# Performance work log

Hardware: AMD Instinct MI355X
Metric: run time of the kernel (lower is better)

Reference implementation:

```python
import jax, jax.numpy as jnp
import numpy as np

MAX_PER_CLASS = 100   # max_num_boxes_per_class
MAX_TOTAL = 300       # max_num_boxes (pad_per_class=False -> output size is MAX_TOTAL)
IOU_THR = 0.5
SCORE_THR = 0.001
NEG = jnp.float32(-1e30)
EPS = 1e-12


def _canon(b):
    # boxes given as any diagonal pair (y1,x1,y2,x2); canonicalize like TF NMS
    ymin = jnp.minimum(b[..., 0], b[..., 2])
    ymax = jnp.maximum(b[..., 0], b[..., 2])
    xmin = jnp.minimum(b[..., 1], b[..., 3])
    xmax = jnp.maximum(b[..., 1], b[..., 3])
    return ymin, xmin, ymax, xmax


def _iou_one_vs_all(box, boxes):
    # box [4], boxes [N,4] -> iou [N]
    y1a, x1a, y2a, x2a = _canon(box)
    y1b, x1b, y2b, x2b = _canon(boxes)
    ih = jnp.maximum(jnp.minimum(y2a, y2b) - jnp.maximum(y1a, y1b), 0.0)
    iw = jnp.maximum(jnp.minimum(x2a, x2b) - jnp.maximum(x1a, x1b), 0.0)
    inter = ih * iw
    area_a = (y2a - y1a) * (x2a - x1a)
    area_b = (y2b - y1b) * (x2b - x1b)
    union = jnp.maximum(area_a + area_b - inter, EPS)
    return inter / union


def _nms_single_class(boxes_c, scores_c):
    # boxes_c [N,4], scores_c [N] -> (scores [K], boxes [K,4], valid [K]) with K=MAX_PER_CLASS
    N = scores_c.shape[0]
    valid = scores_c > SCORE_THR
    s = jnp.where(valid, scores_c, NEG)
    order = jnp.argsort(-s)
    b_sorted = boxes_c[order]          # [N,4]
    s_sorted = s[order]                # [N]
    v_sorted = valid[order]            # [N]

    def step(keep, xs):
        i, box_i, valid_i = xs
        iou_row = _iou_one_vs_all(box_i, b_sorted)          # [N]
        suppressed = jnp.any(keep & (iou_row > IOU_THR))    # vs previously kept only
        keep = keep.at[i].set(valid_i & jnp.logical_not(suppressed))
        return keep, None

    keep0 = jnp.zeros((N,), dtype=bool)
    keep, _ = jax.lax.scan(step, keep0, (jnp.arange(N), b_sorted, v_sorted))

    # cap number of kept boxes at MAX_PER_CLASS (in descending score order)
    rank = jnp.cumsum(keep.astype(jnp.int32)) - 1
    keep = keep & (rank < MAX_PER_CLASS)

    key = jnp.where(keep, s_sorted, NEG)
    top_s, top_i = jax.lax.top_k(key, MAX_PER_CLASS)
    top_boxes = b_sorted[top_i]
    top_valid = top_s > (NEG / 2)
    return top_s, top_boxes, top_valid


def _combined_nms(scores, boxes):
    # scores [B,N,C], boxes [B,N,q,4] with q==1 (boxes shared across classes)
    B, N, C = scores.shape
    q = boxes.shape[2]

    def per_image(scores_i, boxes_i):
        # scores_i [N,C], boxes_i [N,q,4]
        if q == 1:
            cls_boxes = jnp.broadcast_to(boxes_i, (N, C, 4))
        else:
            cls_boxes = boxes_i
        # per-class NMS, vmapped over the class axis
        sc, bx, vd = jax.vmap(_nms_single_class, in_axes=(1, 1))(cls_boxes, scores_i)
        # sc [C,K], bx [C,K,4], vd [C,K]
        cls_ids = jnp.broadcast_to(
            jnp.arange(C, dtype=scores.dtype)[:, None], vd.shape)

        flat_s = jnp.where(vd, sc, NEG).reshape(-1)   # [C*K]
        flat_b = bx.reshape(-1, 4)
        flat_c = cls_ids.reshape(-1)
        flat_v = vd.reshape(-1)

        top_s, idx = jax.lax.top_k(flat_s, MAX_TOTAL)
        out_v = flat_v[idx]
        out_s = jnp.where(out_v, top_s, 0.0)
        out_b = jnp.where(out_v[:, None], flat_b[idx], 0.0)
        out_b = jnp.clip(out_b, 0.0, 1.0)             # clip_boxes=True
        out_c = jnp.where(out_v, flat_c[idx], 0.0)
        count = jnp.sum(out_v.astype(jnp.int32))
        return out_s, out_b, out_c, count

    return jax.vmap(per_image)(scores, boxes)


def setup_inputs() -> dict:
    key = jax.random.key(0)
    k1, k2 = jax.random.split(key)
    B, N, C, Q = 4, 1024, 80, 1
    scores = jax.random.uniform(k1, (B, N, C), dtype=jnp.float32)
    boxes = jax.random.uniform(k2, (B, N, Q, 4), dtype=jnp.float32)
    return {"scores": scores, "boxes": boxes}


def reference(scores, boxes):
    # returns (output_scores, output_boxes, output_classes, valid_counts)
    return _combined_nms(scores, boxes)
```

## Files before the change

### kernel.cpp

```cpp
#include <hip/hip_runtime.h>
#include <stdint.h>

#define N_BOX 1024
#define C_CLS 80
#define B_IMG 4
#define K_PER 100
#define K_TOT 300
#define NEGF  (-1e30f)
#define NWORD 16
#define NCAND (C_CLS * K_PER)
#define M_SEL 8192
#define KPAD  1088

#define OFF_SCOREST 0
#define OFF_MASKS   1310720
#define OFF_WSCORE  1835008
#define OFF_WSIDX   1963008

typedef unsigned long long u64;
typedef unsigned int u32;

__device__ __forceinline__ int swz(int i) { return i + (i >> 4); }

__device__ __forceinline__ u32 ford(float f) {
    u32 u = __float_as_uint(f);
    return (u & 0x80000000u) ? ~u : (u | 0x80000000u);
}
__device__ __forceinline__ float funord(u32 o) {
    u32 u = (o & 0x80000000u) ? (o ^ 0x80000000u) : ~o;
    return __uint_as_float(u);
}

__global__ __launch_bounds__(256) void prep_kernel(
        const float* __restrict__ scores,
        const float* __restrict__ boxes,
        u64*   __restrict__ masks,
        float* __restrict__ scoresT)
{
    __shared__ float4 bx[N_BOX];
    __shared__ float  ar[N_BOX];
    const int tid = threadIdx.x;

    if (blockIdx.x < 256) {
        const int b  = blockIdx.x >> 6;
        const int rg = blockIdx.x & 63;
        for (int n = tid; n < N_BOX; n += 256) {
            float4 v = ((const float4*)boxes)[b * N_BOX + n];
            {
#pragma clang fp contract(off)
                float y1 = fminf(v.x, v.z), y2 = fmaxf(v.x, v.z);
                float x1 = fminf(v.y, v.w), x2 = fmaxf(v.y, v.w);
                bx[n] = make_float4(y1, x1, y2, x2);
                ar[n] = (y2 - y1) * (x2 - x1);
            }
        }
        __syncthreads();

        const int r = tid >> 4;
        const int w = tid & 15;
        const int i = rg * 16 + r;
        const float4 a = bx[i];
        const float area_a = ar[i];
        u64 m = 0;
        const int j0 = w * 64;
        for (int jj = 0; jj < 64; ++jj) {
            int j = j0 + jj;
            float4 q = bx[j];
            {
#pragma clang fp contract(off)
                float ih = fminf(a.z, q.z) - fmaxf(a.x, q.x); ih = fmaxf(ih, 0.0f);
                float iw = fminf(a.w, q.w) - fmaxf(a.y, q.y); iw = fmaxf(iw, 0.0f);
                float inter = ih * iw;
                float uni = fmaxf(area_a + ar[j] - inter, 1e-12f);
                if (j != i && (inter / uni) > 0.5f) m |= (1ull << jj);
            }
        }
        masks[((size_t)(b * N_BOX + i)) * NWORD + w] = m;
    } else {
        float* tile = (float*)bx;
        const int t = blockIdx.x - 256;
        const int b  = t / 320;
        const int rm = t % 320;
        const int n0 = (rm / 5) * 16;
        const int c0 = (rm % 5) * 16;
        const int r = tid >> 4, cc = tid & 15;
        tile[r * 17 + cc] = scores[(size_t)(b * N_BOX + n0 + r) * C_CLS + c0 + cc];
        __syncthreads();
        scoresT[(size_t)(b * C_CLS + c0 + r) * N_BOX + n0 + cc] = tile[cc * 17 + r];
    }
}

__global__ __launch_bounds__(512) void nms_classes(
        const float* __restrict__ scoresT,
        const u64*   __restrict__ masks,
        float* __restrict__ ws_score,
        int*   __restrict__ ws_idx)
{
    __shared__ u64 key[2][KPAD];
    __shared__ u64 rows[2][64][NWORD];
    __shared__ int kept_t[2][K_PER];
    __shared__ int sh_nvalid[2], sh_kept[2];

    const int tid  = threadIdx.x;
    const int half = tid >> 8;
    const int lt   = tid & 255;
    const int lane = tid & 63;
    const int b  = blockIdx.x / (C_CLS / 2);
    const int c  = (blockIdx.x % (C_CLS / 2)) * 2 + half;

    if (lt == 0) { sh_nvalid[half] = 0; sh_kept[half] = 0; }
    __syncthreads();

    u64 r[4];
    {
        const float4 s4 = ((const float4*)(scoresT + ((size_t)(b * C_CLS + c) << 10)))[lt];
        float sv[4] = {s4.x, s4.y, s4.z, s4.w};
        int lv = 0;
        #pragma unroll
        for (int q = 0; q < 4; ++q) {
            bool valid = sv[q] > 0.001f;
            float s = valid ? sv[q] : NEGF;
            int v = lt * 4 + q;
            r[q] = ((u64)ford(s) << 32) | (u32)(N_BOX - 1 - v);
            lv += valid ? 1 : 0;
        }
        if (lv) atomicAdd(&sh_nvalid[half], lv);
    }

    #define CE(a, b, d) { u64 _mx = (a) > (b) ? (a) : (b); \
                          u64 _mn = (a) > (b) ? (b) : (a); \
                          (a) = (d) ? _mx : _mn; (b) = (d) ? _mn : _mx; }
    CE(r[0], r[1], true); CE(r[2], r[3], false);

    for (int k = 4; k <= N_BOX; k <<= 1) {
        const bool d = ((lt & (k >> 2)) == 0);
        for (int j = k >> 1; j > 0; j >>= 1) {
            if (j >= 256) {
                __syncthreads();
                #pragma unroll
                for (int q = 0; q < 4; ++q) key[half][swz(lt * 4 + q)] = r[q];
                __syncthreads();
                const bool upper = ((lt * 4) & j) != 0;
                #pragma unroll
                for (int q = 0; q < 4; ++q) {
                    u64 pv = key[half][swz((lt * 4 + q) ^ j)];
                    u64 mx = r[q] > pv ? r[q] : pv;
                    u64 mn = r[q] > pv ? pv : r[q];
                    r[q] = (d != upper) ? mx : mn;
                }
            } else if (j >= 4) {
                const int dl = j >> 2;
                const bool upper = (lane & dl) != 0;
                #pragma unroll
                for (int q = 0; q < 4; ++q) {
                    u64 pv = __shfl_xor(r[q], dl);
                    u64 mx = r[q] > pv ? r[q] : pv;
                    u64 mn = r[q] > pv ? pv : r[q];
                    r[q] = (d != upper) ? mx : mn;
                }
            } else if (j == 2) {
                CE(r[0], r[2], d); CE(r[1], r[3], d);
            } else {
                CE(r[0], r[1], d); CE(r[2], r[3], d);
            }
        }
    }
    #undef CE

    __syncthreads();
    #pragma unroll
    for (int q = 0; q < 4; ++q) key[half][swz(lt * 4 + q)] = r[q];
    __syncthreads();

    const int wv = tid >> 6;
    if (wv == 0 || wv == 4) {
        const int gh = wv >> 2;
        const int w16 = lane & 15;
        const int sslot = lane >> 4;
        const u64* mrow = masks + (size_t)b * N_BOX * NWORD;
        const int nvalid = sh_nvalid[gh];
        const int nwin = (nvalid + 63) >> 6;
        u64 sup = 0;
        int kept = 0;

        u64 pf[16];
        {
            u64 kv0 = key[gh][swz(lane)];
            int idx0 = (N_BOX - 1) - (int)(u32)(kv0 & 0xFFFFFFFFu);
            #pragma unroll
            for (int p = 0; p < 16; ++p) {
                int rr = p * 4 + sslot;
                int ir = __shfl(idx0, rr);
                pf[p] = (rr < nvalid) ? mrow[(size_t)ir * NWORD + w16] : 0;
            }
        }

        for (int w = 0; w < nwin && kept < K_PER; ++w) {
            const int bt = w * 64;
            #pragma unroll
            for (int p = 0; p < 16; ++p)
                rows[gh][p * 4 + sslot][w16] = pf[p];
            __builtin_amdgcn_wave_barrier();

            if (w + 1 < nwin) {
                u64 kvn = key[gh][swz(bt + 64 + lane)];
                int idxn = (N_BOX - 1) - (int)(u32)(kvn & 0xFFFFFFFFu);
                #pragma unroll
                for (int p = 0; p < 16; ++p) {
                    int rr = p * 4 + sslot;
                    int ir = __shfl(idxn, rr);
                    pf[p] = ((bt + 64 + rr) < nvalid)
                          ? mrow[(size_t)ir * NWORD + w16] : 0;
                }
            }

            int t = bt + lane;
            bool in = t < nvalid;
            u64 kv = key[gh][swz(t & (N_BOX - 1))];
            int idx = (N_BOX - 1) - (int)(u32)(kv & 0xFFFFFFFFu);
            const int widx = idx >> 6, bidx = idx & 63;

            u64 supw = __shfl(sup, widx);
            u64 pending = __ballot(in && !((supw >> bidx) & 1ull));
            if (!pending) continue;

            u64 kill_mask = 0;
            #pragma unroll
            for (int rr = 0; rr < 64; ++rr) {
                u64 wj = rows[gh][rr][widx];
                kill_mask |= ((wj >> bidx) & 1ull) << rr;
            }

            while (pending && kept < K_PER) {
                int t0 = __ffsll((long long)pending) - 1;
                if (lane == 0) kept_t[gh][kept] = bt + t0;
                kept++;
                if (lane < NWORD) sup |= rows[gh][t0][w16];
                bool kill = (kill_mask >> t0) & 1ull;
                pending &= ~(1ull << t0);
                pending &= ~__ballot(kill);
            }
        }
        if (lane == 0) sh_kept[gh] = kept;
    }
    __syncthreads();

    const int kept = sh_kept[half];
    if (lt < K_PER) {
        int ob = (b * C_CLS + c) * K_PER + lt;
        if (lt < kept) {
            u64 k = key[half][swz(kept_t[half][lt])];
            ws_score[ob] = funord((u32)(k >> 32));
            ws_idx[ob]   = (N_BOX - 1) - (int)(u32)(k & 0xFFFFFFFFu);
        } else {
            ws_score[ob] = NEGF;
            ws_idx[ob]   = 0;
        }
    }
}

__global__ __launch_bounds__(1024) void final_topk(
        const float* __restrict__ ws_score,
        const int*   __restrict__ ws_idx,
        const float* __restrict__ boxes,
        float* __restrict__ out)
{
    __shared__ u32 skey[NCAND];
    __shared__ u32 hist4[256 * 4];
    __shared__ u64 list[512];
    __shared__ int sh_sel;
    __shared__ u32 sh_need;
    __shared__ int sh_cnt, sh_valid;

    const int tid = threadIdx.x;
    const int b = blockIdx.x;
    const int base = b * NCAND;

    if (tid == 0) { sh_cnt = 0; sh_valid = 0; }
    for (int i = tid; i < NCAND; i += 1024)
        skey[i] = ford(ws_score[base + i]);
    if (tid < 512) list[tid] = 0;
    hist4[tid] = 0;
    __syncthreads();

    u64 prefix = 0;
    u32 need = K_TOT;
    const int rounds[6] = {7, 6, 5, 4, 1, 0};
    const int slot = tid & 3;

    for (int rd = 0; rd < 6; ++rd) {
        const int d = rounds[rd];
        for (int i = tid; i < NCAND; i += 1024) {
            u64 k = ((u64)skey[i] << 32) | (u32)(M_SEL - 1 - i);
            bool match = (d == 7) || (((k ^ prefix) >> (8 * (d + 1))) == 0);
            if (match)
                atomicAdd(&hist4[(((u32)(k >> (8 * d)) & 0xFFu) << 2) | slot], 1u);
        }
        __syncthreads();
        if (tid < 64) {
            const int l = tid;
            u32 h[4];
            #pragma unroll
            for (int q = 0; q < 4; ++q) {
                int bin = 4 * l + q;
                h[q] = hist4[bin * 4 + 0] + hist4[bin * 4 + 1]
                     + hist4[bin * 4 + 2] + hist4[bin * 4 + 3];
                hist4[bin * 4 + 0] = 0; hist4[bin * 4 + 1] = 0;
                hist4[bin * 4 + 2] = 0; hist4[bin * 4 + 3] = 0;
            }
            u32 s3 = h[3], s2 = h[2] + s3, s1 = h[1] + s2, s0 = h[0] + s1;
            u32 tot = s0, S = tot;
            #pragma unroll
            for (int off = 1; off < 64; off <<= 1) {
                u32 t = __shfl(S, (l + off) & 63);
                if (l + off < 64) S += t;
            }
            u32 T = S - tot;
            u32 sv0 = s0 + T, sv1 = s1 + T, sv2 = s2 + T, sv3 = s3 + T;
            if (sv0 >= need && sv1 < need) { sh_sel = 4*l;     sh_need = need - sv1; }
            if (sv1 >= need && sv2 < need) { sh_sel = 4*l + 1; sh_need = need - sv2; }
            if (sv2 >= need && sv3 < need) { sh_sel = 4*l + 2; sh_need = need - sv3; }
            if (sv3 >= need && T   < need) { sh_sel = 4*l + 3; sh_need = need - T;   }
        }
        __syncthreads();
        prefix |= ((u64)(u32)sh_sel) << (8 * d);
        need = sh_need;
        __syncthreads();
    }

    for (int i = tid; i < NCAND; i += 1024) {
        u64 k = ((u64)skey[i] << 32) | (u32)(M_SEL - 1 - i);
        if (k >= prefix) {
            int p = atomicAdd(&sh_cnt, 1);
            if (p < 512) list[p] = k;
        }
    }
    __syncthreads();

    if (tid < 64) {
        const int l = tid;
        u64 e[8];
        #pragma unroll
        for (int q = 0; q < 8; ++q) e[q] = list[l * 8 + q];
        #define CE2(a, b, dd) { u64 _mx = (a) > (b) ? (a) : (b); \
                                u64 _mn = (a) > (b) ? (b) : (a); \
                                (a) = (dd) ? _mx : _mn; (b) = (dd) ? _mn : _mx; }
        CE2(e[0], e[1], true);  CE2(e[2], e[3], false);
        CE2(e[4], e[5], true);  CE2(e[6], e[7], false);
        CE2(e[0], e[2], true);  CE2(e[1], e[3], true);
        CE2(e[4], e[6], false); CE2(e[5], e[7], false);
        CE2(e[0], e[1], true);  CE2(e[2], e[3], true);
        CE2(e[4], e[5], false); CE2(e[6], e[7], false);
        for (int k = 8; k <= 512; k <<= 1) {
            const bool d = ((l & (k >> 3)) == 0);
            for (int j = k >> 1; j >= 8; j >>= 1) {
                const int dl = j >> 3;
                const bool upper = (l & dl) != 0;
                #pragma unroll
                for (int q = 0; q < 8; ++q) {
                    u64 pv = __shfl_xor(e[q], dl);
                    u64 mx = e[q] > pv ? e[q] : pv;
                    u64 mn = e[q] > pv ? pv : e[q];
                    e[q] = (d != upper) ? mx : mn;
                }
            }
            CE2(e[0], e[4], d); CE2(e[1], e[5], d);
            CE2(e[2], e[6], d); CE2(e[3], e[7], d);
            CE2(e[0], e[2], d); CE2(e[1], e[3], d);
            CE2(e[4], e[6], d); CE2(e[5], e[7], d);
            CE2(e[0], e[1], d); CE2(e[2], e[3], d);
            CE2(e[4], e[5], d); CE2(e[6], e[7], d);
        }
        #undef CE2
        #pragma unroll
        for (int q = 0; q < 8; ++q) list[l * 8 + q] = e[q];
    }
    __syncthreads();

    float* out_s = out;
    float* out_b = out + B_IMG * K_TOT;
    float* out_c = out + B_IMG * K_TOT * 5;
    float* out_n = out + B_IMG * K_TOT * 6;

    for (int i = tid; i < K_TOT; i += 1024) {
        u64 k = list[i];
        float s = funord((u32)(k >> 32));
        int flat = (M_SEL - 1) - (int)(u32)(k & 0xFFFFFFFFu);
        bool valid = s > (-5e29f);
        float os = 0.0f, oc = 0.0f;
        float4 ob = make_float4(0.0f, 0.0f, 0.0f, 0.0f);
        if (valid && flat < NCAND) {
            int cc = flat / K_PER;
            int n  = ws_idx[base + flat];
            float4 bb = ((const float4*)boxes)[b * N_BOX + n];
            os = s;
            oc = (float)cc;
            ob.x = fminf(fmaxf(bb.x, 0.0f), 1.0f);
            ob.y = fminf(fmaxf(bb.y, 0.0f), 1.0f);
            ob.z = fminf(fmaxf(bb.z, 0.0f), 1.0f);
            ob.w = fminf(fmaxf(bb.w, 0.0f), 1.0f);
            atomicAdd(&sh_valid, 1);
        }
        out_s[b * K_TOT + i] = os;
        ((float4*)out_b)[b * K_TOT + i] = ob;
        out_c[b * K_TOT + i] = oc;
    }
    __syncthreads();
    if (tid == 0) out_n[b] = (float)sh_valid;
}

extern "C" void kernel_launch(void* const* d_in, const int* in_sizes, int n_in,
                              void* d_out, int out_size, void* d_ws, size_t ws_size,
                              hipStream_t stream) {
    const float* scores = (const float*)d_in[0];
    const float* boxes  = (const float*)d_in[1];

    char* ws = (char*)d_ws;
    float* scoresT  = (float*)(ws + OFF_SCOREST);
    u64*   masks    = (u64*)  (ws + OFF_MASKS);
    float* ws_score = (float*)(ws + OFF_WSCORE);
    int*   ws_idx   = (int*)  (ws + OFF_WSIDX);

    prep_kernel<<<dim3(256 + 1280), dim3(256), 0, stream>>>(scores, boxes, masks, scoresT);
    nms_classes<<<dim3(B_IMG * (C_CLS / 2)), dim3(512), 0, stream>>>(
        scoresT, masks, ws_score, ws_idx);
    final_topk<<<dim3(B_IMG), dim3(1024), 0, stream>>>(
        ws_score, ws_idx, boxes, (float*)d_out);
}
```

Before: 121.8 us.

## Drop precomputed IoU mask kernel; compute IoU on the fly in per-class NMS

Removes the prep kernel that built a full 1024x1024 IoU bitmask per image and transposed the scores. The NMS kernel now loads the boxes into shared memory, reads scores with a class stride, and computes IoU directly: each candidate is checked against the already-kept boxes, and the intra-window kill masks are computed per window. This removes one launch and the mask traffic in exchange for more arithmetic inside the serial NMS wave and uncoalesced strided score reads.

```diff
diff --git a/kernel.cpp b/kernel.cpp
--- a/kernel.cpp
+++ b/kernel.cpp
@@ -7,13 +7,10 @@
 #define K_PER 100
 #define K_TOT 300
 #define NEGF  (-1e30f)
-#define NWORD 16
 #define NCAND (C_CLS * K_PER)
 #define M_SEL 8192
 #define KPAD  1088
 
-#define OFF_SCOREST 0
-#define OFF_MASKS   1310720
 #define OFF_WSCORE  1835008
 #define OFF_WSIDX   1963008
 
@@ -31,75 +28,21 @@
     return __uint_as_float(u);
 }
 
-__global__ __launch_bounds__(256) void prep_kernel(
+__global__ __launch_bounds__(512, 2) void nms_classes(
         const float* __restrict__ scores,
         const float* __restrict__ boxes,
-        u64*   __restrict__ masks,
-        float* __restrict__ scoresT)
-{
-    __shared__ float4 bx[N_BOX];
-    __shared__ float  ar[N_BOX];
-    const int tid = threadIdx.x;
-
-    if (blockIdx.x < 256) {
-        const int b  = blockIdx.x >> 6;
-        const int rg = blockIdx.x & 63;
-        for (int n = tid; n < N_BOX; n += 256) {
-            float4 v = ((const float4*)boxes)[b * N_BOX + n];
-            {
-#pragma clang fp contract(off)
-                float y1 = fminf(v.x, v.z), y2 = fmaxf(v.x, v.z);
-                float x1 = fminf(v.y, v.w), x2 = fmaxf(v.y, v.w);
-                bx[n] = make_float4(y1, x1, y2, x2);
-                ar[n] = (y2 - y1) * (x2 - x1);
-            }
-        }
-        __syncthreads();
-
-        const int r = tid >> 4;
-        const int w = tid & 15;
-        const int i = rg * 16 + r;
-        const float4 a = bx[i];
-        const float area_a = ar[i];
-        u64 m = 0;
-        const int j0 = w * 64;
-        for (int jj = 0; jj < 64; ++jj) {
-            int j = j0 + jj;
-            float4 q = bx[j];
-            {
-#pragma clang fp contract(off)
-                float ih = fminf(a.z, q.z) - fmaxf(a.x, q.x); ih = fmaxf(ih, 0.0f);
-                float iw = fminf(a.w, q.w) - fmaxf(a.y, q.y); iw = fmaxf(iw, 0.0f);
-                float inter = ih * iw;
-                float uni = fmaxf(area_a + ar[j] - inter, 1e-12f);
-                if (j != i && (inter / uni) > 0.5f) m |= (1ull << jj);
-            }
-        }
-        masks[((size_t)(b * N_BOX + i)) * NWORD + w] = m;
-    } else {
-        float* tile = (float*)bx;
-        const int t = blockIdx.x - 256;
-        const int b  = t / 320;
-        const int rm = t % 320;
-        const int n0 = (rm / 5) * 16;
-        const int c0 = (rm % 5) * 16;
-        const int r = tid >> 4, cc = tid & 15;
-        tile[r * 17 + cc] = scores[(size_t)(b * N_BOX + n0 + r) * C_CLS + c0 + cc];
-        __syncthreads();
-        scoresT[(size_t)(b * C_CLS + c0 + r) * N_BOX + n0 + cc] = tile[cc * 17 + r];
-    }
-}
-
-__global__ __launch_bounds__(512) void nms_classes(
-        const float* __restrict__ scoresT,
-        const u64*   __restrict__ masks,
         float* __restrict__ ws_score,
         int*   __restrict__ ws_idx)
 {
-    __shared__ u64 key[2][KPAD];
-    __shared__ u64 rows[2][64][NWORD];
-    __shared__ int kept_t[2][K_PER];
-    __shared__ int sh_nvalid[2], sh_kept[2];
+    __shared__ u64    key[2][KPAD];
+    __shared__ float4 bx[N_BOX];
+    __shared__ float  ar[N_BOX];
+    __shared__ float4 wb[2][64];
+    __shared__ float  wa[2][64];
+    __shared__ float4 kb[2][K_PER];
+    __shared__ float  ka[2][K_PER];
+    __shared__ int    kept_t[2][K_PER];
+    __shared__ int    sh_nvalid[2], sh_kept[2];
 
     const int tid  = threadIdx.x;
     const int half = tid >> 8;
@@ -109,18 +52,29 @@
     const int c  = (blockIdx.x % (C_CLS / 2)) * 2 + half;
 
     if (lt == 0) { sh_nvalid[half] = 0; sh_kept[half] = 0; }
+
+    for (int n = tid; n < N_BOX; n += 512) {
+        float4 v = ((const float4*)boxes)[b * N_BOX + n];
+        {
+#pragma clang fp contract(off)
+            float y1 = fminf(v.x, v.z), y2 = fmaxf(v.x, v.z);
+            float x1 = fminf(v.y, v.w), x2 = fmaxf(v.y, v.w);
+            bx[n] = make_float4(y1, x1, y2, x2);
+            ar[n] = (y2 - y1) * (x2 - x1);
+        }
+    }
     __syncthreads();
 
     u64 r[4];
     {
-        const float4 s4 = ((const float4*)(scoresT + ((size_t)(b * C_CLS + c) << 10)))[lt];
-        float sv[4] = {s4.x, s4.y, s4.z, s4.w};
+        const float* sc = scores + (size_t)(b * N_BOX) * C_CLS + c;
         int lv = 0;
         #pragma unroll
         for (int q = 0; q < 4; ++q) {
-            bool valid = sv[q] > 0.001f;
-            float s = valid ? sv[q] : NEGF;
             int v = lt * 4 + q;
+            float s0 = sc[(size_t)v * C_CLS];
+            bool valid = s0 > 0.001f;
+            float s = valid ? s0 : NEGF;
             r[q] = ((u64)ford(s) << 32) | (u32)(N_BOX - 1 - v);
             lv += valid ? 1 : 0;
         }
@@ -175,67 +129,58 @@
     const int wv = tid >> 6;
     if (wv == 0 || wv == 4) {
         const int gh = wv >> 2;
-        const int w16 = lane & 15;
-        const int sslot = lane >> 4;
-        const u64* mrow = masks + (size_t)b * N_BOX * NWORD;
         const int nvalid = sh_nvalid[gh];
         const int nwin = (nvalid + 63) >> 6;
-        u64 sup = 0;
         int kept = 0;
-
-        u64 pf[16];
-        {
-            u64 kv0 = key[gh][swz(lane)];
-            int idx0 = (N_BOX - 1) - (int)(u32)(kv0 & 0xFFFFFFFFu);
-            #pragma unroll
-            for (int p = 0; p < 16; ++p) {
-                int rr = p * 4 + sslot;
-                int ir = __shfl(idx0, rr);
-                pf[p] = (rr < nvalid) ? mrow[(size_t)ir * NWORD + w16] : 0;
-            }
-        }
 
         for (int w = 0; w < nwin && kept < K_PER; ++w) {
             const int bt = w * 64;
-            #pragma unroll
-            for (int p = 0; p < 16; ++p)
-                rows[gh][p * 4 + sslot][w16] = pf[p];
-            __builtin_amdgcn_wave_barrier();
-
-            if (w + 1 < nwin) {
-                u64 kvn = key[gh][swz(bt + 64 + lane)];
-                int idxn = (N_BOX - 1) - (int)(u32)(kvn & 0xFFFFFFFFu);
-                #pragma unroll
-                for (int p = 0; p < 16; ++p) {
-                    int rr = p * 4 + sslot;
-                    int ir = __shfl(idxn, rr);
-                    pf[p] = ((bt + 64 + rr) < nvalid)
-                          ? mrow[(size_t)ir * NWORD + w16] : 0;
-                }
-            }
-
-            int t = bt + lane;
-            bool in = t < nvalid;
+            const int t = bt + lane;
+            const bool in = t < nvalid;
             u64 kv = key[gh][swz(t & (N_BOX - 1))];
             int idx = (N_BOX - 1) - (int)(u32)(kv & 0xFFFFFFFFu);
-            const int widx = idx >> 6, bidx = idx & 63;
-
-            u64 supw = __shfl(sup, widx);
-            u64 pending = __ballot(in && !((supw >> bidx) & 1ull));
+            const float4 q4 = bx[idx];
+            const float  aq = ar[idx];
+
+            bool alive = in;
+            for (int k = 0; k < kept; ++k) {
+                float4 p = kb[gh][k];
+                float ap = ka[gh][k];
+                {
+#pragma clang fp contract(off)
+                    float ih = fminf(p.z, q4.z) - fmaxf(p.x, q4.x); ih = fmaxf(ih, 0.0f);
+                    float iw = fminf(p.w, q4.w) - fmaxf(p.y, q4.y); iw = fmaxf(iw, 0.0f);
+                    float inter = ih * iw;
+                    float uni = fmaxf(ap + aq - inter, 1e-12f);
+                    if ((inter / uni) > 0.5f) alive = false;
+                }
+            }
+            u64 pending = __ballot(alive);
             if (!pending) continue;
 
+            wb[gh][lane] = q4; wa[gh][lane] = aq;
+            __builtin_amdgcn_wave_barrier();
             u64 kill_mask = 0;
-            #pragma unroll
             for (int rr = 0; rr < 64; ++rr) {
-                u64 wj = rows[gh][rr][widx];
-                kill_mask |= ((wj >> bidx) & 1ull) << rr;
+                float4 p = wb[gh][rr];
+                float ap = wa[gh][rr];
+                bool kill;
+                {
+#pragma clang fp contract(off)
+                    float ih = fminf(p.z, q4.z) - fmaxf(p.x, q4.x); ih = fmaxf(ih, 0.0f);
+                    float iw = fminf(p.w, q4.w) - fmaxf(p.y, q4.y); iw = fmaxf(iw, 0.0f);
+                    float inter = ih * iw;
+                    float uni = fmaxf(ap + aq - inter, 1e-12f);
+                    kill = (rr != lane) && ((inter / uni) > 0.5f);
+                }
+                kill_mask |= ((u64)kill) << rr;
             }
 
             while (pending && kept < K_PER) {
                 int t0 = __ffsll((long long)pending) - 1;
                 if (lane == 0) kept_t[gh][kept] = bt + t0;
+                if (lane == t0) { kb[gh][kept] = q4; ka[gh][kept] = aq; }
                 kept++;
-                if (lane < NWORD) sup |= rows[gh][t0][w16];
                 bool kill = (kill_mask >> t0) & 1ull;
                 pending &= ~(1ull << t0);
                 pending &= ~__ballot(kill);
@@ -416,14 +361,11 @@
     const float* boxes  = (const float*)d_in[1];
 
     char* ws = (char*)d_ws;
-    float* scoresT  = (float*)(ws + OFF_SCOREST);
-    u64*   masks    = (u64*)  (ws + OFF_MASKS);
     float* ws_score = (float*)(ws + OFF_WSCORE);
     int*   ws_idx   = (int*)  (ws + OFF_WSIDX);
 
-    prep_kernel<<<dim3(256 + 1280), dim3(256), 0, stream>>>(scores, boxes, masks, scoresT);
     nms_classes<<<dim3(B_IMG * (C_CLS / 2)), dim3(512), 0, stream>>>(
-        scoresT, masks, ws_score, ws_idx);
+        scores, boxes, ws_score, ws_idx);
     final_topk<<<dim3(B_IMG), dim3(1024), 0, stream>>>(
         ws_score, ws_idx, boxes, (float*)d_out);
 }
```

After: 145.9 us. 19.7% more time.
